# Kernel optimization log

Measured on AMD Instinct MI355X. Metric: run time of the kernel, lower is better.

The kernel has to match this reference:

```python
import jax, jax.numpy as jnp
import numpy as np
import math

N_NODES = 50000
N_EDGES = 800000
D = 128        # in_channels == out_channels
H = 8          # num_heads
HD = D // H    # head_dim = 16
ED = 32        # edge_dim


def setup_inputs() -> dict:
    key = jax.random.key(0)
    ks = jax.random.split(key, 16)
    s = 1.0 / math.sqrt(D)
    se = 1.0 / math.sqrt(ED)
    return {
        "x": jax.random.normal(ks[0], (N_NODES, D), jnp.float32),
        "edge_index": jax.random.randint(ks[1], (2, N_EDGES), 0, N_NODES, jnp.int64),
        "edge_attr": jax.random.normal(ks[2], (N_EDGES, ED), jnp.float32),
        "Wq": jax.random.normal(ks[3], (D, D), jnp.float32) * s,
        "bq": jnp.zeros((D,), jnp.float32),
        "Wk": jax.random.normal(ks[4], (D, D), jnp.float32) * s,
        "bk": jnp.zeros((D,), jnp.float32),
        "Wv": jax.random.normal(ks[5], (D, D), jnp.float32) * s,
        "bv": jnp.zeros((D,), jnp.float32),
        "We": jax.random.normal(ks[6], (ED, H), jnp.float32) * se,
        "be": jnp.zeros((H,), jnp.float32),
        "Wo": jax.random.normal(ks[7], (D, D), jnp.float32) * s,
        "bo": jnp.zeros((D,), jnp.float32),
        "gamma": jnp.ones((D,), jnp.float32),
        "beta": jnp.zeros((D,), jnp.float32),
    }


def reference(x, edge_index, edge_attr, Wq, bq, Wk, bk, Wv, bv, We, be, Wo, bo, gamma, beta):
    n = x.shape[0]
    residual = x
    # node-wise projections -> [N, H, HD]
    q = (x @ Wq + bq).reshape(n, H, HD)
    k = (x @ Wk + bk).reshape(n, H, HD)
    v = (x @ Wv + bv).reshape(n, H, HD)
    src = edge_index[0]
    dst = edge_index[1]
    # edge-wise gather + dot-product attention score [E, H]
    score = jnp.einsum('ehd,ehd->eh', q[dst], k[src]) / math.sqrt(HD)
    score = score + edge_attr @ We + be
    # segmented (per-destination-node) stable softmax
    m = jax.ops.segment_max(score, dst, num_segments=n)          # [N, H]
    exp_s = jnp.exp(score - m[dst])                              # [E, H]
    ssum = jax.ops.segment_sum(exp_s, dst, num_segments=n)      # [N, H]
    attn = exp_s / (ssum[dst] + 1e-8)                            # [E, H]
    # weighted message scatter-add
    msg = attn[..., None] * v[src]                               # [E, H, HD]
    out = jax.ops.segment_sum(msg, dst, num_segments=n)          # [N, H, HD]
    out = out.reshape(n, D) @ Wo + bo
    # residual + layer norm (eps=1e-5, as nn.LayerNorm default)
    h = out + residual
    mu = h.mean(-1, keepdims=True)
    var = ((h - mu) ** 2).mean(-1, keepdims=True)
    return (h - mu) / jnp.sqrt(var + 1e-5) * gamma + beta
```

## Files before the change

### kernel.cpp

```cpp
#include <hip/hip_runtime.h>

#define DD 128
#define HH 8
#define HDIM 16
#define EDIM 32
#define CAP 44
#define RECB 24

typedef short short8_t __attribute__((ext_vector_type(8)));
typedef float f32x4 __attribute__((ext_vector_type(4)));

__device__ inline ushort f2bf(float f) {
    unsigned u = __float_as_uint(f);
    unsigned r = (u + 0x7fffu + ((u >> 16) & 1u)) >> 16;
    return (ushort)r;
}
__device__ inline float bf2f(ushort u) { return __uint_as_float(((unsigned)u) << 16); }

__global__ __launch_bounds__(256) void k_prep_w(
    const float* __restrict__ Wq, const float* __restrict__ Wk,
    const float* __restrict__ Wv, const float* __restrict__ Wo,
    ushort* __restrict__ wt, int* __restrict__ cnt, int N)
{
    const int t = threadIdx.x;
    if (blockIdx.x >= 4) {
        int i = (blockIdx.x - 4) * 256 + t;
        if (i < N) cnt[i] = 0;
        return;
    }
    __shared__ ushort tw[128][136];
    const float* Ws[4] = {Wq, Wk, Wv, Wo};
    const float* W = Ws[blockIdx.x];
    for (int idx = t; idx < DD * DD; idx += 256) {
        int k = idx >> 7, c = idx & 127;
        tw[c][k] = f2bf(W[idx]);
    }
    __syncthreads();
    for (int u = t; u < 2048; u += 256) {
        int col = u >> 4, c8 = (u & 15) * 8;
        *(uint4*)&wt[((size_t)blockIdx.x * 128 + col) * 128 + c8] = *(const uint4*)&tw[col][c8];
    }
}

__global__ __launch_bounds__(256) void k_qkv(
    const float* __restrict__ x, const ushort* __restrict__ wt,
    const float* __restrict__ bq, const float* __restrict__ bk, const float* __restrict__ bv,
    ushort* __restrict__ qb, ushort* __restrict__ kv, int N)
{
    __shared__ ushort xs[64][136];
    const int t = threadIdx.x;
    const int base = blockIdx.x * 64;

    for (int u = t; u < 1024; u += 256) {
        int r = u >> 4, c8 = (u & 15) * 8;
        int n = base + r;
        if (n < N) {
            float4 a = *(const float4*)&x[(size_t)n * DD + c8];
            float4 b = *(const float4*)&x[(size_t)n * DD + c8 + 4];
            ushort o[8] = {f2bf(a.x), f2bf(a.y), f2bf(a.z), f2bf(a.w),
                           f2bf(b.x), f2bf(b.y), f2bf(b.z), f2bf(b.w)};
            *(uint4*)&xs[r][c8] = *(const uint4*)o;
        } else {
            *(uint4*)&xs[r][c8] = make_uint4(0u, 0u, 0u, 0u);
        }
    }
    __syncthreads();

    const int lane = t & 63, w = t >> 6;
    const int lr = lane & 15, g = lane >> 4;
    const int node = base + w * 16 + lr;
    const bool valid = node < N;

    short8_t xf[4];
    #pragma unroll
    for (int ks = 0; ks < 4; ++ks)
        xf[ks] = *(const short8_t*)&xs[w * 16 + lr][ks * 32 + g * 8];

    const float* biases[3] = {bq, bk, bv};
    #pragma unroll
    for (int m = 0; m < 3; ++m) {
        f32x4 acc[8];
        #pragma unroll
        for (int rt = 0; rt < 8; ++rt) acc[rt] = (f32x4){0.f, 0.f, 0.f, 0.f};
        #pragma unroll
        for (int ks = 0; ks < 4; ++ks) {
            #pragma unroll
            for (int rt = 0; rt < 8; ++rt) {
                short8_t wf = *(const short8_t*)&wt[((size_t)m * 128 + rt * 16 + lr) * 128 + ks * 32 + g * 8];
                acc[rt] = __builtin_amdgcn_mfma_f32_16x16x32_bf16(wf, xf[ks], acc[rt], 0, 0, 0);
            }
        }
        if (valid) {
            #pragma unroll
            for (int rt = 0; rt < 8; ++rt) {
                int col = rt * 16 + g * 4;
                float4 b4 = *(const float4*)&biases[m][col];
                ushort o[4] = {f2bf(acc[rt][0] + b4.x), f2bf(acc[rt][1] + b4.y),
                               f2bf(acc[rt][2] + b4.z), f2bf(acc[rt][3] + b4.w)};
                if (m == 0) *(uint2*)&qb[(size_t)node * DD + col] = *(const uint2*)o;
                else        *(uint2*)&kv[(size_t)node * 256 + (m == 1 ? 0 : 128) + col] = *(const uint2*)o;
            }
        }
    }
}

__global__ __launch_bounds__(256) void k_edge(
    const int* __restrict__ ei, const float* __restrict__ edge_attr,
    const float* __restrict__ We, const float* __restrict__ be,
    int E, int N, int* __restrict__ cnt, char* __restrict__ peb)
{
    __shared__ float wel[EDIM * HH];
    __shared__ float bel[HH];
    const int t = threadIdx.x;
    for (int i = t; i < EDIM * HH; i += 256) wel[i] = We[i];
    if (t < HH) bel[t] = be[t];
    __syncthreads();

    int e = blockIdx.x * 256 + t;
    if (e >= E) return;
    int dst = ei[E + e];
    int src = ei[e];

    int pos = -1;
    if ((unsigned)dst < (unsigned)N) pos = atomicAdd(&cnt[dst], 1);

    float acc[HH];
    #pragma unroll
    for (int h = 0; h < HH; ++h) acc[h] = bel[h];
    #pragma unroll
    for (int c = 0; c < EDIM; c += 4) {
        float4 a4 = *(const float4*)&edge_attr[(size_t)e * EDIM + c];
        float av[4] = {a4.x, a4.y, a4.z, a4.w};
        #pragma unroll
        for (int cc = 0; cc < 4; ++cc)
            #pragma unroll
            for (int h = 0; h < HH; ++h)
                acc[h] += av[cc] * wel[(c + cc) * HH + h];
    }

    if (pos >= 0 && pos < CAP) {
        unsigned d[6];
        d[0] = (unsigned)(((unsigned)src < (unsigned)N) ? src : 0);
        #pragma unroll
        for (int i = 0; i < 4; ++i)
            d[1 + i] = (unsigned)f2bf(acc[2*i]) | ((unsigned)f2bf(acc[2*i + 1]) << 16);
        d[5] = 0u;
        char* p = peb + ((size_t)dst * CAP + pos) * RECB;
        *(unsigned long long*)(p)      = (unsigned long long)d[0] | ((unsigned long long)d[1] << 32);
        *(unsigned long long*)(p + 8)  = (unsigned long long)d[2] | ((unsigned long long)d[3] << 32);
        *(unsigned long long*)(p + 16) = (unsigned long long)d[4] | ((unsigned long long)d[5] << 32);
    }
}

__global__ __launch_bounds__(256) void k_agg(
    const ushort* __restrict__ qb, const ushort* __restrict__ kv,
    const int* __restrict__ cnt, const char* __restrict__ peb,
    ushort* __restrict__ aggb, int N)
{
    int node = blockIdx.x * 4 + (threadIdx.x >> 6);
    if (node >= N) return;
    int lane = threadIdx.x & 63;
    int h = lane & 7, j = lane >> 3;

    float qr[HDIM];
    {
        uint4 qa = *(const uint4*)&qb[(size_t)node * DD + h * 16];
        uint4 qc = *(const uint4*)&qb[(size_t)node * DD + h * 16 + 8];
        unsigned ua[4] = {qa.x, qa.y, qa.z, qa.w};
        unsigned ub[4] = {qc.x, qc.y, qc.z, qc.w};
        #pragma unroll
        for (int i = 0; i < 4; ++i) {
            qr[2*i]     = __uint_as_float(ua[i] << 16);
            qr[2*i + 1] = __uint_as_float(ua[i] & 0xffff0000u);
            qr[8 + 2*i]     = __uint_as_float(ub[i] << 16);
            qr[8 + 2*i + 1] = __uint_as_float(ub[i] & 0xffff0000u);
        }
    }

    int deg = cnt[node];
    if (deg > CAP) deg = CAP;
    const char* pbase = peb + (size_t)node * CAP * RECB;

    float acc[HDIM];
    #pragma unroll
    for (int d = 0; d < HDIM; ++d) acc[d] = 0.f;
    float denom = 0.f;

    int tt = j;
    for (; tt + 8 < deg; tt += 16) {
        const char* p0 = pbase + (size_t)tt * RECB;
        const char* p1 = pbase + (size_t)(tt + 8) * RECB;
        int s0 = *(const int*)p0;
        int s1 = *(const int*)p1;
        float e0 = bf2f(*(const ushort*)(p0 + 4 + 2 * h));
        float e1 = bf2f(*(const ushort*)(p1 + 4 + 2 * h));
        const uint4* kp0 = (const uint4*)&kv[(size_t)s0 * 256 + h * 16];
        const uint4* kp1 = (const uint4*)&kv[(size_t)s1 * 256 + h * 16];
        uint4 ka0 = kp0[0], kb0 = kp0[1];
        uint4 ka1 = kp1[0], kb1 = kp1[1];
        const uint4* vp0 = (const uint4*)&kv[(size_t)s0 * 256 + 128 + h * 16];
        const uint4* vp1 = (const uint4*)&kv[(size_t)s1 * 256 + 128 + h * 16];
        uint4 va0 = vp0[0], vb0 = vp0[1];
        uint4 va1 = vp1[0], vb1 = vp1[1];

        float kf0[16], kf1[16], vf0[16], vf1[16];
        {
            unsigned ua[4] = {ka0.x, ka0.y, ka0.z, ka0.w};
            unsigned ub[4] = {kb0.x, kb0.y, kb0.z, kb0.w};
            #pragma unroll
            for (int i = 0; i < 4; ++i) {
                kf0[2*i]     = __uint_as_float(ua[i] << 16);
                kf0[2*i + 1] = __uint_as_float(ua[i] & 0xffff0000u);
                kf0[8 + 2*i]     = __uint_as_float(ub[i] << 16);
                kf0[8 + 2*i + 1] = __uint_as_float(ub[i] & 0xffff0000u);
            }
        }
        {
            unsigned ua[4] = {ka1.x, ka1.y, ka1.z, ka1.w};
            unsigned ub[4] = {kb1.x, kb1.y, kb1.z, kb1.w};
            #pragma unroll
            for (int i = 0; i < 4; ++i) {
                kf1[2*i]     = __uint_as_float(ua[i] << 16);
                kf1[2*i + 1] = __uint_as_float(ua[i] & 0xffff0000u);
                kf1[8 + 2*i]     = __uint_as_float(ub[i] << 16);
                kf1[8 + 2*i + 1] = __uint_as_float(ub[i] & 0xffff0000u);
            }
        }
        {
            unsigned ua[4] = {va0.x, va0.y, va0.z, va0.w};
            unsigned ub[4] = {vb0.x, vb0.y, vb0.z, vb0.w};
            #pragma unroll
            for (int i = 0; i < 4; ++i) {
                vf0[2*i]     = __uint_as_float(ua[i] << 16);
                vf0[2*i + 1] = __uint_as_float(ua[i] & 0xffff0000u);
                vf0[8 + 2*i]     = __uint_as_float(ub[i] << 16);
                vf0[8 + 2*i + 1] = __uint_as_float(ub[i] & 0xffff0000u);
            }
        }
        {
            unsigned ua[4] = {va1.x, va1.y, va1.z, va1.w};
            unsigned ub[4] = {vb1.x, vb1.y, vb1.z, vb1.w};
            #pragma unroll
            for (int i = 0; i < 4; ++i) {
                vf1[2*i]     = __uint_as_float(ua[i] << 16);
                vf1[2*i + 1] = __uint_as_float(ua[i] & 0xffff0000u);
                vf1[8 + 2*i]     = __uint_as_float(ub[i] << 16);
                vf1[8 + 2*i + 1] = __uint_as_float(ub[i] & 0xffff0000u);
            }
        }
        float qk0 = 0.f, qk1 = 0.f;
        #pragma unroll
        for (int d = 0; d < HDIM; ++d) { qk0 += qr[d] * kf0[d]; qk1 += qr[d] * kf1[d]; }
        float w0 = __expf(e0 + qk0 * 0.25f);
        float w1 = __expf(e1 + qk1 * 0.25f);
        denom += w0 + w1;
        #pragma unroll
        for (int d = 0; d < HDIM; ++d) acc[d] += w0 * vf0[d] + w1 * vf1[d];
    }
    if (tt < deg) {
        const char* p0 = pbase + (size_t)tt * RECB;
        int s0 = *(const int*)p0;
        float e0 = bf2f(*(const ushort*)(p0 + 4 + 2 * h));
        const uint4* kp0 = (const uint4*)&kv[(size_t)s0 * 256 + h * 16];
        uint4 ka0 = kp0[0], kb0 = kp0[1];
        const uint4* vp0 = (const uint4*)&kv[(size_t)s0 * 256 + 128 + h * 16];
        uint4 va0 = vp0[0], vb0 = vp0[1];
        float kf0[16], vf0[16];
        {
            unsigned ua[4] = {ka0.x, ka0.y, ka0.z, ka0.w};
            unsigned ub[4] = {kb0.x, kb0.y, kb0.z, kb0.w};
            #pragma unroll
            for (int i = 0; i < 4; ++i) {
                kf0[2*i]     = __uint_as_float(ua[i] << 16);
                kf0[2*i + 1] = __uint_as_float(ua[i] & 0xffff0000u);
                kf0[8 + 2*i]     = __uint_as_float(ub[i] << 16);
                kf0[8 + 2*i + 1] = __uint_as_float(ub[i] & 0xffff0000u);
            }
        }
        {
            unsigned ua[4] = {va0.x, va0.y, va0.z, va0.w};
            unsigned ub[4] = {vb0.x, vb0.y, vb0.z, vb0.w};
            #pragma unroll
            for (int i = 0; i < 4; ++i) {
                vf0[2*i]     = __uint_as_float(ua[i] << 16);
                vf0[2*i + 1] = __uint_as_float(ua[i] & 0xffff0000u);
                vf0[8 + 2*i]     = __uint_as_float(ub[i] << 16);
                vf0[8 + 2*i + 1] = __uint_as_float(ub[i] & 0xffff0000u);
            }
        }
        float qk0 = 0.f;
        #pragma unroll
        for (int d = 0; d < HDIM; ++d) qk0 += qr[d] * kf0[d];
        float w0 = __expf(e0 + qk0 * 0.25f);
        denom += w0;
        #pragma unroll
        for (int d = 0; d < HDIM; ++d) acc[d] += w0 * vf0[d];
    }

    #pragma unroll
    for (int m = 8; m < 64; m <<= 1) {
        denom += __shfl_xor(denom, m, 64);
        #pragma unroll
        for (int d = 0; d < HDIM; ++d) acc[d] += __shfl_xor(acc[d], m, 64);
    }

    if (j == 0) {
        float inv = 1.f / (denom + 1e-8f);
        unsigned uu[8];
        #pragma unroll
        for (int i = 0; i < 8; ++i) {
            unsigned lo = f2bf(acc[2*i] * inv);
            unsigned hi = f2bf(acc[2*i + 1] * inv);
            uu[i] = lo | (hi << 16);
        }
        *(uint4*)&aggb[(size_t)node * DD + h * 16]     = *(const uint4*)&uu[0];
        *(uint4*)&aggb[(size_t)node * DD + h * 16 + 8] = *(const uint4*)&uu[4];
    }
}

__global__ __launch_bounds__(256) void k_final(
    const ushort* __restrict__ aggb, const ushort* __restrict__ wto,
    const float* __restrict__ x, const float* __restrict__ bo,
    const float* __restrict__ gamma, const float* __restrict__ beta,
    float* __restrict__ out, int N)
{
    __shared__ ushort as_[64][136];
    const int t = threadIdx.x;
    const int base = blockIdx.x * 64;

    for (int u = t; u < 1024; u += 256) {
        int r = u >> 4, c8 = (u & 15) * 8;
        int n = base + r;
        uint4 val = (n < N) ? *(const uint4*)&aggb[(size_t)n * DD + c8] : make_uint4(0u, 0u, 0u, 0u);
        *(uint4*)&as_[r][c8] = val;
    }
    __syncthreads();

    const int lane = t & 63, w = t >> 6;
    const int lr = lane & 15, g = lane >> 4;
    const int node = base + w * 16 + lr;
    const bool valid = node < N;

    short8_t af[4];
    #pragma unroll
    for (int ks = 0; ks < 4; ++ks)
        af[ks] = *(const short8_t*)&as_[w * 16 + lr][ks * 32 + g * 8];

    f32x4 acc[8];
    #pragma unroll
    for (int rt = 0; rt < 8; ++rt) acc[rt] = (f32x4){0.f, 0.f, 0.f, 0.f};
    #pragma unroll
    for (int ks = 0; ks < 4; ++ks) {
        #pragma unroll
        for (int rt = 0; rt < 8; ++rt) {
            short8_t wf = *(const short8_t*)&wto[((size_t)rt * 16 + lr) * 128 + ks * 32 + g * 8];
            acc[rt] = __builtin_amdgcn_mfma_f32_16x16x32_bf16(wf, af[ks], acc[rt], 0, 0, 0);
        }
    }

    float s = 0.f, sq = 0.f;
    #pragma unroll
    for (int rt = 0; rt < 8; ++rt) {
        int col = rt * 16 + g * 4;
        float4 b4 = *(const float4*)&bo[col];
        float4 xr = valid ? *(const float4*)&x[(size_t)node * DD + col] : make_float4(0.f, 0.f, 0.f, 0.f);
        float y0 = acc[rt][0] + b4.x + xr.x;
        float y1 = acc[rt][1] + b4.y + xr.y;
        float y2 = acc[rt][2] + b4.z + xr.z;
        float y3 = acc[rt][3] + b4.w + xr.w;
        acc[rt][0] = y0; acc[rt][1] = y1; acc[rt][2] = y2; acc[rt][3] = y3;
        s += y0 + y1 + y2 + y3;
        sq += y0 * y0 + y1 * y1 + y2 * y2 + y3 * y3;
    }
    s  += __shfl_xor(s, 16, 64);  sq += __shfl_xor(sq, 16, 64);
    s  += __shfl_xor(s, 32, 64);  sq += __shfl_xor(sq, 32, 64);

    float mu = s * (1.f / 128.f);
    float var = sq * (1.f / 128.f) - mu * mu;
    float rstd = rsqrtf(var + 1e-5f);

    if (valid) {
        #pragma unroll
        for (int rt = 0; rt < 8; ++rt) {
            int col = rt * 16 + g * 4;
            float4 g4 = *(const float4*)&gamma[col];
            float4 e4 = *(const float4*)&beta[col];
            float4 o;
            o.x = (acc[rt][0] - mu) * rstd * g4.x + e4.x;
            o.y = (acc[rt][1] - mu) * rstd * g4.y + e4.y;
            o.z = (acc[rt][2] - mu) * rstd * g4.z + e4.z;
            o.w = (acc[rt][3] - mu) * rstd * g4.w + e4.w;
            *(float4*)&out[(size_t)node * DD + col] = o;
        }
    }
}

extern "C" void kernel_launch(void* const* d_in, const int* in_sizes, int n_in,
                              void* d_out, int out_size, void* d_ws, size_t ws_size,
                              hipStream_t stream) {
    const float* x     = (const float*)d_in[0];
    const int*   ei    = (const int*)d_in[1];
    const float* ea    = (const float*)d_in[2];
    const float* Wq    = (const float*)d_in[3];
    const float* bq    = (const float*)d_in[4];
    const float* Wk    = (const float*)d_in[5];
    const float* bk    = (const float*)d_in[6];
    const float* Wv    = (const float*)d_in[7];
    const float* bv    = (const float*)d_in[8];
    const float* We    = (const float*)d_in[9];
    const float* be    = (const float*)d_in[10];
    const float* Wo    = (const float*)d_in[11];
    const float* bo    = (const float*)d_in[12];
    const float* gamma = (const float*)d_in[13];
    const float* beta  = (const float*)d_in[14];
    float* out = (float*)d_out;

    const int N = in_sizes[0] / DD;
    const int E = in_sizes[2] / EDIM;

    char*   peb  = (char*)d_ws;
    ushort* qb   = (ushort*)(peb + (size_t)N * CAP * RECB);
    ushort* kv   = qb + (size_t)N * DD;
    ushort* aggb = kv + (size_t)N * 256;
    ushort* wt   = aggb + (size_t)N * DD;
    int*    cnt  = (int*)(wt + 4 * 128 * 128);

    const int nodeTiles64 = (N + 63) / 64;
    const int edgeBlocks  = (E + 255) / 256;
    const int aggBlocks   = (N + 3) / 4;
    const int prepBlocks  = 4 + (N + 255) / 256;

    k_prep_w<<<prepBlocks, 256, 0, stream>>>(Wq, Wk, Wv, Wo, wt, cnt, N);
    k_qkv<<<nodeTiles64, 256, 0, stream>>>(x, wt, bq, bk, bv, qb, kv, N);
    k_edge<<<edgeBlocks, 256, 0, stream>>>(ei, ea, We, be, E, N, cnt, peb);
    k_agg<<<aggBlocks, 256, 0, stream>>>(qb, kv, cnt, peb, aggb, N);
    k_final<<<nodeTiles64, 256, 0, stream>>>(aggb, wt + 3 * 128 * 128, x, bo, gamma, beta, out, N);
}
```

Measured before the change: 212.9 us.

## Interleave K/V per head and split edge records into SoA arrays

Stores K and V for each head next to each other in the kv buffer, so each lane gathers one contiguous 64-byte run per source node instead of two separate 32-byte runs. The packed 24-byte per-edge record becomes two arrays: source indices, plus 16-byte aligned edge-score vectors written with a single vector store. This is meant to cut scattered gather transactions in the aggregation kernel and avoid misaligned record stores. It adds a second workspace array and changes the addressing used by both the write and read sides.

Result: slower. 250.3 us (+17.6%).

```diff
diff --git a/kernel.cpp b/kernel.cpp
--- a/kernel.cpp
+++ b/kernel.cpp
@@ -5,7 +5,6 @@
 #define HDIM 16
 #define EDIM 32
 #define CAP 44
-#define RECB 24
 
 typedef short short8_t __attribute__((ext_vector_type(8)));
 typedef float f32x4 __attribute__((ext_vector_type(4)));
@@ -97,8 +96,10 @@
                 float4 b4 = *(const float4*)&biases[m][col];
                 ushort o[4] = {f2bf(acc[rt][0] + b4.x), f2bf(acc[rt][1] + b4.y),
                                f2bf(acc[rt][2] + b4.z), f2bf(acc[rt][3] + b4.w)};
-                if (m == 0) *(uint2*)&qb[(size_t)node * DD + col] = *(const uint2*)o;
-                else        *(uint2*)&kv[(size_t)node * 256 + (m == 1 ? 0 : 128) + col] = *(const uint2*)o;
+                if (m == 0)
+                    *(uint2*)&qb[(size_t)node * DD + col] = *(const uint2*)o;
+                else
+                    *(uint2*)&kv[(size_t)node * 256 + rt * 32 + (m == 1 ? 0 : 16) + g * 4] = *(const uint2*)o;
             }
         }
     }
@@ -107,7 +108,8 @@
 __global__ __launch_bounds__(256) void k_edge(
     const int* __restrict__ ei, const float* __restrict__ edge_attr,
     const float* __restrict__ We, const float* __restrict__ be,
-    int E, int N, int* __restrict__ cnt, char* __restrict__ peb)
+    int E, int N, int* __restrict__ cnt,
+    int* __restrict__ srcs, ushort* __restrict__ esc)
 {
     __shared__ float wel[EDIM * HH];
     __shared__ float bel[HH];
@@ -139,22 +141,20 @@
     }
 
     if (pos >= 0 && pos < CAP) {
-        unsigned d[6];
-        d[0] = (unsigned)(((unsigned)src < (unsigned)N) ? src : 0);
+        size_t slot = (size_t)dst * CAP + pos;
+        srcs[slot] = ((unsigned)src < (unsigned)N) ? src : 0;
+        unsigned d[4];
         #pragma unroll
         for (int i = 0; i < 4; ++i)
-            d[1 + i] = (unsigned)f2bf(acc[2*i]) | ((unsigned)f2bf(acc[2*i + 1]) << 16);
-        d[5] = 0u;
-        char* p = peb + ((size_t)dst * CAP + pos) * RECB;
-        *(unsigned long long*)(p)      = (unsigned long long)d[0] | ((unsigned long long)d[1] << 32);
-        *(unsigned long long*)(p + 8)  = (unsigned long long)d[2] | ((unsigned long long)d[3] << 32);
-        *(unsigned long long*)(p + 16) = (unsigned long long)d[4] | ((unsigned long long)d[5] << 32);
+            d[i] = (unsigned)f2bf(acc[2*i]) | ((unsigned)f2bf(acc[2*i + 1]) << 16);
+        *(uint4*)&esc[slot * 8] = *(const uint4*)d;
     }
 }
 
 __global__ __launch_bounds__(256) void k_agg(
     const ushort* __restrict__ qb, const ushort* __restrict__ kv,
-    const int* __restrict__ cnt, const char* __restrict__ peb,
+    const int* __restrict__ cnt, const int* __restrict__ srcs,
+    const ushort* __restrict__ esc,
     ushort* __restrict__ aggb, int N)
 {
     int node = blockIdx.x * 4 + (threadIdx.x >> 6);
@@ -179,7 +179,7 @@
 
     int deg = cnt[node];
     if (deg > CAP) deg = CAP;
-    const char* pbase = peb + (size_t)node * CAP * RECB;
+    const size_t base = (size_t)node * CAP;
 
     float acc[HDIM];
     #pragma unroll
@@ -188,20 +188,16 @@
 
     int tt = j;
     for (; tt + 8 < deg; tt += 16) {
-        const char* p0 = pbase + (size_t)tt * RECB;
-        const char* p1 = pbase + (size_t)(tt + 8) * RECB;
-        int s0 = *(const int*)p0;
-        int s1 = *(const int*)p1;
-        float e0 = bf2f(*(const ushort*)(p0 + 4 + 2 * h));
-        float e1 = bf2f(*(const ushort*)(p1 + 4 + 2 * h));
-        const uint4* kp0 = (const uint4*)&kv[(size_t)s0 * 256 + h * 16];
-        const uint4* kp1 = (const uint4*)&kv[(size_t)s1 * 256 + h * 16];
-        uint4 ka0 = kp0[0], kb0 = kp0[1];
-        uint4 ka1 = kp1[0], kb1 = kp1[1];
-        const uint4* vp0 = (const uint4*)&kv[(size_t)s0 * 256 + 128 + h * 16];
-        const uint4* vp1 = (const uint4*)&kv[(size_t)s1 * 256 + 128 + h * 16];
-        uint4 va0 = vp0[0], vb0 = vp0[1];
-        uint4 va1 = vp1[0], vb1 = vp1[1];
+        int s0 = srcs[base + tt];
+        int s1 = srcs[base + tt + 8];
+        float e0 = bf2f(esc[(base + tt) * 8 + h]);
+        float e1 = bf2f(esc[(base + tt + 8) * 8 + h]);
+        const ushort* kvb0 = &kv[(size_t)s0 * 256 + h * 32];
+        const ushort* kvb1 = &kv[(size_t)s1 * 256 + h * 32];
+        uint4 ka0 = *(const uint4*)(kvb0),      kb0 = *(const uint4*)(kvb0 + 8);
+        uint4 va0 = *(const uint4*)(kvb0 + 16), vb0 = *(const uint4*)(kvb0 + 24);
+        uint4 ka1 = *(const uint4*)(kvb1),      kb1 = *(const uint4*)(kvb1 + 8);
+        uint4 va1 = *(const uint4*)(kvb1 + 16), vb1 = *(const uint4*)(kvb1 + 24);
 
         float kf0[16], kf1[16], vf0[16], vf1[16];
         {
@@ -258,13 +254,11 @@
         for (int d = 0; d < HDIM; ++d) acc[d] += w0 * vf0[d] + w1 * vf1[d];
     }
     if (tt < deg) {
-        const char* p0 = pbase + (size_t)tt * RECB;
-        int s0 = *(const int*)p0;
-        float e0 = bf2f(*(const ushort*)(p0 + 4 + 2 * h));
-        const uint4* kp0 = (const uint4*)&kv[(size_t)s0 * 256 + h * 16];
-        uint4 ka0 = kp0[0], kb0 = kp0[1];
-        const uint4* vp0 = (const uint4*)&kv[(size_t)s0 * 256 + 128 + h * 16];
-        uint4 va0 = vp0[0], vb0 = vp0[1];
+        int s0 = srcs[base + tt];
+        float e0 = bf2f(esc[(base + tt) * 8 + h]);
+        const ushort* kvb0 = &kv[(size_t)s0 * 256 + h * 32];
+        uint4 ka0 = *(const uint4*)(kvb0),      kb0 = *(const uint4*)(kvb0 + 8);
+        uint4 va0 = *(const uint4*)(kvb0 + 16), vb0 = *(const uint4*)(kvb0 + 24);
         float kf0[16], vf0[16];
         {
             unsigned ua[4] = {ka0.x, ka0.y, ka0.z, ka0.w};
@@ -418,8 +412,9 @@
     const int N = in_sizes[0] / DD;
     const int E = in_sizes[2] / EDIM;
 
-    char*   peb  = (char*)d_ws;
-    ushort* qb   = (ushort*)(peb + (size_t)N * CAP * RECB);
+    ushort* esc  = (ushort*)d_ws;
+    int*    srcs = (int*)(esc + (size_t)N * CAP * 8);
+    ushort* qb   = (ushort*)(srcs + (size_t)N * CAP);
     ushort* kv   = qb + (size_t)N * DD;
     ushort* aggb = kv + (size_t)N * 256;
     ushort* wt   = aggb + (size_t)N * DD;
@@ -432,7 +427,7 @@
 
     k_prep_w<<<prepBlocks, 256, 0, stream>>>(Wq, Wk, Wv, Wo, wt, cnt, N);
     k_qkv<<<nodeTiles64, 256, 0, stream>>>(x, wt, bq, bk, bv, qb, kv, N);
-    k_edge<<<edgeBlocks, 256, 0, stream>>>(ei, ea, We, be, E, N, cnt, peb);
-    k_agg<<<aggBlocks, 256, 0, stream>>>(qb, kv, cnt, peb, aggb, N);
+    k_edge<<<edgeBlocks, 256, 0, stream>>>(ei, ea, We, be, E, N, cnt, srcs, esc);
+    k_agg<<<aggBlocks, 256, 0, stream>>>(qb, kv, cnt, srcs, esc, aggb, N);
     k_final<<<nodeTiles64, 256, 0, stream>>>(aggb, wt + 3 * 128 * 128, x, bo, gamma, beta, out, N);
 }
```
